# Performance work log

Measured on AMD Instinct MI355X. Metric: run time of the kernel, lower is better.

Reference implementation:

```python
import jax, jax.numpy as jnp
import numpy as np

B, N, F, T = 32, 2048, 64, 24


def setup_inputs() -> dict:
    key = jax.random.key(0)
    ks = jax.random.split(key, 6)
    x = jax.random.normal(ks[0], (B, N, F, T), dtype=jnp.float32)
    # glorot-uniform-ish init scales
    def glorot(k, shape):
        fan_in, fan_out = shape[-2], shape[-1]
        lim = (6.0 / (fan_in + fan_out)) ** 0.5
        return jax.random.uniform(k, shape, jnp.float32, -lim, lim)
    W1 = glorot(ks[1], (T, 1))
    W2 = glorot(ks[2], (F, T))
    W3 = glorot(ks[3], (1, F))
    bs = glorot(ks[4], (1, N, N))
    Vs = glorot(ks[5], (N, N))
    return {"x": x, "W1": W1, "W2": W2, "W3": W3, "bs": bs, "Vs": Vs}


def reference(x, W1, W2, W3, bs, Vs):
    # x: (B, N, F, T)
    # lhs = squeeze(x @ W1, -1) @ W2  -> (B, N, T)
    lhs = jnp.einsum('bnft,t->bnf', x, W1[:, 0])          # (B,N,F)
    lhs = jnp.einsum('bnf,ft->bnt', lhs, W2)              # (B,N,T)
    # rhs = transpose(squeeze(W3 @ x, 2), (0,2,1)) -> (B, T, N)
    rhs = jnp.einsum('f,bnft->btn', W3[0], x)             # (B,T,N)
    product = jnp.einsum('bnt,btm->bnm', lhs, rhs)        # (B,N,N)
    S = jnp.einsum('nk,bkm->bnm', Vs, jax.nn.sigmoid(product + bs))  # (B,N,N)
    # softmax over axis 1 (rows of the N x N map)
    return jax.nn.softmax(S, axis=1)
```

## Files before the change

kernel.cpp:

```cpp
#include <hip/hip_runtime.h>

constexpr int Bc = 32, Nc = 2048, Fc = 64, Tc = 24;

__device__ __forceinline__ unsigned short f2bf(float f) {
  unsigned u = __float_as_uint(f);
  u += 0x7fffu + ((u >> 16) & 1u);
  return (unsigned short)(u >> 16);
}

#define AS1(p) ((const __attribute__((address_space(1))) unsigned int*)(p))
#define AS3(p) ((__attribute__((address_space(3))) unsigned int*)(p))

typedef __attribute__((ext_vector_type(8))) short bfrag;
typedef __attribute__((ext_vector_type(4))) float ffrag;

__global__ __launch_bounds__(256) void kA(const float* __restrict__ x,
                                          const float* __restrict__ W1,
                                          const float* __restrict__ W2,
                                          const float* __restrict__ W3,
                                          float* __restrict__ lhs,
                                          float* __restrict__ rhsT) {
  __shared__ float W2s[Fc * Tc];
  __shared__ float xs[4][Fc][26];
  __shared__ float tmp[4][Fc];
  const int tid = threadIdx.x;
  for (int i = tid; i < Fc * Tc; i += 256) W2s[i] = W2[i];
  const int wave = tid >> 6, lane = tid & 63;
  const size_t pair = (size_t)blockIdx.x * 4 + wave;
  const float* xp = x + pair * (size_t)(Fc * Tc);
#pragma unroll
  for (int s = 0; s < 12; ++s) {
    int f2 = lane + 64 * s;
    int row = f2 / 12, c2 = (f2 % 12) * 2;
    float2 v = *(const float2*)(xp + (size_t)f2 * 2);
    xs[wave][row][c2] = v.x;
    xs[wave][row][c2 + 1] = v.y;
  }
  __syncthreads();
  {
    const int f = lane;
    float acc = 0.f;
#pragma unroll
    for (int t = 0; t < Tc; ++t) acc += xs[wave][f][t] * W1[t];
    tmp[wave][f] = acc;
  }
  __syncthreads();
  if (lane < 48) {
    const int t = lane >> 1, h = lane & 1;
    const int f0 = h * 32;
    float lacc = 0.f, racc = 0.f;
#pragma unroll
    for (int i = 0; i < 32; ++i) {
      int f = f0 + i;
      lacc += tmp[wave][f] * W2s[f * Tc + t];
      racc += W3[f] * xs[wave][f][t];
    }
    lacc += __shfl_xor(lacc, 1);
    racc += __shfl_xor(racc, 1);
    if (h == 0) {
      lhs[pair * Tc + t] = lacc;
      rhsT[pair * Tc + t] = racc;
    }
  }
}

__global__ __launch_bounds__(256) void kVs(const float* __restrict__ Vs,
                                           unsigned short* __restrict__ Vb) {
  size_t i = ((size_t)blockIdx.x * 256 + threadIdx.x) * 4;
  float4 v = *(const float4*)(Vs + i);
  ushort4 o;
  o.x = f2bf(v.x); o.y = f2bf(v.y); o.z = f2bf(v.z); o.w = f2bf(v.w);
  *(ushort4*)(Vb + i) = o;
}

__global__ __launch_bounds__(256) void kP(const float* __restrict__ lhs,
                                          const float* __restrict__ rhsT,
                                          const float* __restrict__ bsr,
                                          unsigned short* __restrict__ sigT) {
  __shared__ float Lt[Tc][132];
  __shared__ float Rt[Tc][132];
  const int b = blockIdx.z;
  const int i0 = blockIdx.y * 128;
  const int j0 = blockIdx.x * 128;
  const int tid = threadIdx.x;
  const float* lp = lhs + ((size_t)b * Nc + i0) * Tc;
  const float* rp = rhsT + ((size_t)b * Nc + j0) * Tc;
#pragma unroll
  for (int s = 0; s < 6; ++s) {
    int f2 = tid + 256 * s;
    int row = f2 / 12, c2 = (f2 % 12) * 2;
    float2 v = *(const float2*)(lp + (size_t)row * Tc + c2);
    Lt[c2][row] = v.x; Lt[c2 + 1][row] = v.y;
    float2 w = *(const float2*)(rp + (size_t)row * Tc + c2);
    Rt[c2][row] = w.x; Rt[c2 + 1][row] = w.y;
  }
  __syncthreads();
  const int tx = tid & 15, ty = tid >> 4;
  const int ri = ty * 8, cj = tx * 8;
  float acc[8][8];
#pragma unroll
  for (int a = 0; a < 8; ++a) {
    const float* bp = bsr + (size_t)(i0 + ri + a) * Nc + j0 + cj;
    float4 b0 = *(const float4*)bp;
    float4 b1 = *(const float4*)(bp + 4);
    acc[a][0] = b0.x; acc[a][1] = b0.y; acc[a][2] = b0.z; acc[a][3] = b0.w;
    acc[a][4] = b1.x; acc[a][5] = b1.y; acc[a][6] = b1.z; acc[a][7] = b1.w;
  }
#pragma unroll
  for (int t = 0; t < Tc; ++t) {
    float la[8], ra[8];
    *(float4*)&la[0] = *(const float4*)&Lt[t][ri];
    *(float4*)&la[4] = *(const float4*)&Lt[t][ri + 4];
    *(float4*)&ra[0] = *(const float4*)&Rt[t][cj];
    *(float4*)&ra[4] = *(const float4*)&Rt[t][cj + 4];
#pragma unroll
    for (int a = 0; a < 8; ++a)
#pragma unroll
      for (int c = 0; c < 8; ++c) acc[a][c] += la[a] * ra[c];
  }
#pragma unroll
  for (int c = 0; c < 8; ++c) {
    unsigned short o[8];
#pragma unroll
    for (int a = 0; a < 8; ++a) {
      float e = __expf(-acc[a][c]);
      o[a] = f2bf(__fdividef(1.0f, 1.0f + e));
    }
    uint4 pk;
    pk.x = (unsigned)o[0] | ((unsigned)o[1] << 16);
    pk.y = (unsigned)o[2] | ((unsigned)o[3] << 16);
    pk.z = (unsigned)o[4] | ((unsigned)o[5] << 16);
    pk.w = (unsigned)o[6] | ((unsigned)o[7] << 16);
    *(uint4*)(sigT + ((size_t)b * Nc + j0 + cj + c) * Nc + i0 + ri) = pk;
  }
}

__global__ __launch_bounds__(256) void kG(const unsigned short* __restrict__ A,
                                          const unsigned short* __restrict__ Bm,
                                          float* __restrict__ S) {
  __shared__ unsigned short As[128 * 32];
  __shared__ unsigned short Bs[128 * 32];
  const int b = blockIdx.y;
  const int n0 = (blockIdx.x >> 4) << 7;
  const int m0 = (blockIdx.x & 15) << 7;
  const int tid = threadIdx.x;
  const int wave = tid >> 6, lane = tid & 63;
  const int quad = lane >> 4, l16 = lane & 15;
  const int wrow = (wave >> 1) << 6, wcol = (wave & 1) << 6;
  const unsigned short* Bg = Bm + (size_t)b * Nc * Nc;

  ffrag acc[4][4];
#pragma unroll
  for (int i = 0; i < 4; ++i)
#pragma unroll
    for (int j = 0; j < 4; ++j) acc[i][j] = (ffrag){0.f, 0.f, 0.f, 0.f};

  const int part = (lane & 3) * 8;
  const int row0 = (wave << 4) + (lane >> 2);
  const int row1 = row0 + 64;

  for (int kt = 0; kt < Nc / 32; ++kt) {
    const int k0 = kt * 32;
    __builtin_amdgcn_global_load_lds(AS1(A + (size_t)(n0 + row0) * Nc + k0 + part),
                                     AS3(&As[(wave * 64) * 8]), 16, 0, 0);
    __builtin_amdgcn_global_load_lds(AS1(A + (size_t)(n0 + row1) * Nc + k0 + part),
                                     AS3(&As[(256 + wave * 64) * 8]), 16, 0, 0);
    __builtin_amdgcn_global_load_lds(AS1(Bg + (size_t)(m0 + row0) * Nc + k0 + part),
                                     AS3(&Bs[(wave * 64) * 8]), 16, 0, 0);
    __builtin_amdgcn_global_load_lds(AS1(Bg + (size_t)(m0 + row1) * Nc + k0 + part),
                                     AS3(&Bs[(256 + wave * 64) * 8]), 16, 0, 0);
    __syncthreads();
    bfrag af[4], bg[4];
#pragma unroll
    for (int mi = 0; mi < 4; ++mi)
      af[mi] = *(const bfrag*)&As[(wrow + mi * 16 + l16) * 32 + quad * 8];
#pragma unroll
    for (int ni = 0; ni < 4; ++ni)
      bg[ni] = *(const bfrag*)&Bs[(wcol + ni * 16 + l16) * 32 + quad * 8];
#pragma unroll
    for (int mi = 0; mi < 4; ++mi)
#pragma unroll
      for (int ni = 0; ni < 4; ++ni)
        acc[mi][ni] = __builtin_amdgcn_mfma_f32_16x16x32_bf16(af[mi], bg[ni], acc[mi][ni], 0, 0, 0);
    __syncthreads();
  }
  float* Sp = S + (size_t)b * Nc * Nc;
#pragma unroll
  for (int mi = 0; mi < 4; ++mi)
#pragma unroll
    for (int r = 0; r < 4; ++r) {
      const int row = n0 + wrow + mi * 16 + quad * 4 + r;
#pragma unroll
      for (int ni = 0; ni < 4; ++ni)
        Sp[(size_t)row * Nc + (m0 + wcol + ni * 16 + l16)] = acc[mi][ni][r];
    }
}

__global__ __launch_bounds__(256) void kS1(const float* __restrict__ S,
                                           float* __restrict__ pmax,
                                           float* __restrict__ psum) {
  const int b = blockIdx.z, mt = blockIdx.y, nc = blockIdx.x;
  const int m = mt * 256 + threadIdx.x;
  const float* col = S + (size_t)b * Nc * Nc + m;
  float mx = -3.0e38f, sm = 0.f;
  const int ns = nc * 512;
#pragma unroll 4
  for (int n = ns; n < ns + 512; ++n) {
    float v = col[(size_t)n * Nc];
    float nm = fmaxf(mx, v);
    sm = sm * __expf(mx - nm) + __expf(v - nm);
    mx = nm;
  }
  pmax[(size_t)(b * 4 + nc) * Nc + m] = mx;
  psum[(size_t)(b * 4 + nc) * Nc + m] = sm;
}

__global__ __launch_bounds__(256) void kS1b(const float* __restrict__ pmax,
                                            const float* __restrict__ psum,
                                            float* __restrict__ rmax,
                                            float* __restrict__ rinv) {
  const int i = blockIdx.x * 256 + threadIdx.x;
  const int b = i >> 11, m = i & 2047;
  const float* pm = pmax + (size_t)b * 4 * Nc + m;
  const float* ps = psum + (size_t)b * 4 * Nc + m;
  float gm = pm[0];
#pragma unroll
  for (int c = 1; c < 4; ++c) gm = fmaxf(gm, pm[(size_t)c * Nc]);
  float gs = 0.f;
#pragma unroll
  for (int c = 0; c < 4; ++c) gs += ps[(size_t)c * Nc] * __expf(pm[(size_t)c * Nc] - gm);
  rmax[i] = gm;
  rinv[i] = 1.0f / gs;
}

__global__ __launch_bounds__(256) void kS2(float* __restrict__ S,
                                           const float* __restrict__ rmax,
                                           const float* __restrict__ rinv) {
  const int b = blockIdx.z, mt = blockIdx.y, nc = blockIdx.x;
  const int m = mt * 256 + threadIdx.x;
  const float gm = rmax[b * Nc + m];
  const float iv = rinv[b * Nc + m];
  float* col = S + (size_t)b * Nc * Nc + m;
  const int ns = nc * 256;
#pragma unroll 4
  for (int n = ns; n < ns + 256; ++n) {
    float v = col[(size_t)n * Nc];
    col[(size_t)n * Nc] = __expf(v - gm) * iv;
  }
}

extern "C" void kernel_launch(void* const* d_in, const int* in_sizes, int n_in,
                              void* d_out, int out_size, void* d_ws, size_t ws_size,
                              hipStream_t stream) {
  const float* x   = (const float*)d_in[0];
  const float* W1  = (const float*)d_in[1];
  const float* W2  = (const float*)d_in[2];
  const float* W3  = (const float*)d_in[3];
  const float* bsr = (const float*)d_in[4];
  const float* Vs  = (const float*)d_in[5];
  float* out = (float*)d_out;

  char* ws = (char*)d_ws;
  constexpr size_t SIGT_B = (size_t)Bc * Nc * Nc * 2;
  constexpr size_t VB_B   = (size_t)Nc * Nc * 2;
  constexpr size_t LHS_B  = (size_t)Bc * Nc * Tc * 4;
  constexpr size_t PM_B   = (size_t)Bc * 4 * Nc * 4;
  unsigned short* sigT = (unsigned short*)ws;
  unsigned short* Vb   = (unsigned short*)(ws + SIGT_B);
  float* lhs  = (float*)(ws + SIGT_B + VB_B);
  float* rhsT = (float*)(ws + SIGT_B + VB_B + LHS_B);
  float* pmax = (float*)(ws + SIGT_B + VB_B + 2 * LHS_B);
  float* psum = (float*)(ws + SIGT_B + VB_B + 2 * LHS_B + PM_B);
  float* rmax = (float*)(ws + SIGT_B + VB_B + 2 * LHS_B + 2 * PM_B);
  float* rinv = (float*)(ws + SIGT_B + VB_B + 2 * LHS_B + 2 * PM_B + (size_t)Bc * Nc * 4);

  kA<<<Bc * Nc / 4, 256, 0, stream>>>(x, W1, W2, W3, lhs, rhsT);
  kVs<<<(Nc * Nc) / 1024, 256, 0, stream>>>(Vs, Vb);
  kP<<<dim3(Nc / 128, Nc / 128, Bc), 256, 0, stream>>>(lhs, rhsT, bsr, sigT);
  kG<<<dim3((Nc / 128) * (Nc / 128), Bc), 256, 0, stream>>>(Vb, sigT, out);
  kS1<<<dim3(4, Nc / 256, Bc), 256, 0, stream>>>(out, pmax, psum);
  kS1b<<<Bc * Nc / 256, 256, 0, stream>>>(pmax, psum, rmax, rinv);
  kS2<<<dim3(Nc / 256, Nc / 256, Bc), 256, 0, stream>>>(out, rmax, rinv);
}
```

Measured before the change: 2.195 ms.

## Rewrite batched bf16 GEMM as 256x256 double-buffered pipelined MFMA kernel

```diff
diff --git a/kernel.cpp b/kernel.cpp
--- a/kernel.cpp
+++ b/kernel.cpp
@@ -135,65 +135,166 @@
   }
 }
 
-__global__ __launch_bounds__(256) void kG(const unsigned short* __restrict__ A,
-                                          const unsigned short* __restrict__ Bm,
-                                          float* __restrict__ S) {
-  __shared__ unsigned short As[128 * 32];
-  __shared__ unsigned short Bs[128 * 32];
+__global__ __launch_bounds__(512, 2) void kG(const unsigned short* __restrict__ A,
+                                             const unsigned short* __restrict__ Bm,
+                                             float* __restrict__ S) {
+  __shared__ unsigned short As[2][2][8192];
+  __shared__ unsigned short Bs[2][2][8192];
   const int b = blockIdx.y;
-  const int n0 = (blockIdx.x >> 4) << 7;
-  const int m0 = (blockIdx.x & 15) << 7;
+  const int bid = blockIdx.x;
+  const int swz = (bid & 7) * 8 + (bid >> 3);
+  const int n0 = (swz >> 3) << 8;
+  const int m0 = (swz & 7) << 8;
   const int tid = threadIdx.x;
-  const int wave = tid >> 6, lane = tid & 63;
+  const int wid = tid >> 6, lane = tid & 63;
+  const int wm = wid >> 2, wn = wid & 3;
   const int quad = lane >> 4, l16 = lane & 15;
-  const int wrow = (wave >> 1) << 6, wcol = (wave & 1) << 6;
   const unsigned short* Bg = Bm + (size_t)b * Nc * Nc;
 
-  ffrag acc[4][4];
-#pragma unroll
-  for (int i = 0; i < 4; ++i)
-#pragma unroll
-    for (int j = 0; j < 4; ++j) acc[i][j] = (ffrag){0.f, 0.f, 0.f, 0.f};
-
-  const int part = (lane & 3) * 8;
-  const int row0 = (wave << 4) + (lane >> 2);
-  const int row1 = row0 + 64;
-
-  for (int kt = 0; kt < Nc / 32; ++kt) {
-    const int k0 = kt * 32;
-    __builtin_amdgcn_global_load_lds(AS1(A + (size_t)(n0 + row0) * Nc + k0 + part),
-                                     AS3(&As[(wave * 64) * 8]), 16, 0, 0);
-    __builtin_amdgcn_global_load_lds(AS1(A + (size_t)(n0 + row1) * Nc + k0 + part),
-                                     AS3(&As[(256 + wave * 64) * 8]), 16, 0, 0);
-    __builtin_amdgcn_global_load_lds(AS1(Bg + (size_t)(m0 + row0) * Nc + k0 + part),
-                                     AS3(&Bs[(wave * 64) * 8]), 16, 0, 0);
-    __builtin_amdgcn_global_load_lds(AS1(Bg + (size_t)(m0 + row1) * Nc + k0 + part),
-                                     AS3(&Bs[(256 + wave * 64) * 8]), 16, 0, 0);
-    __syncthreads();
-    bfrag af[4], bg[4];
+  int srow[2], scol[2], sbase[2];
+#pragma unroll
+  for (int c = 0; c < 2; ++c) {
+    const int d = c * 8192 + (wid << 10) + (lane << 4);
+    const int q = d ^ (((d >> 9) & 1) << 5);
+    srow[c] = q >> 7;
+    scol[c] = (q & 127) >> 1;
+    sbase[c] = (c * 8192 + (wid << 10)) >> 1;
+  }
+
+#define STAGE(arr, bufb, half, gb, ro, k0)                                         \
+  do {                                                                             \
+    _Pragma("unroll")                                                              \
+    for (int c = 0; c < 2; ++c)                                                    \
+      __builtin_amdgcn_global_load_lds(                                            \
+          AS1(gb + (size_t)((ro) + srow[c]) * Nc + (k0) + scol[c]),                \
+          AS3(&arr[bufb][half][0] + sbase[c]), 16, 0, 0);                          \
+  } while (0)
+
+  ffrag acc[2][4][2][2];
+#pragma unroll
+  for (int qm = 0; qm < 2; ++qm)
 #pragma unroll
     for (int mi = 0; mi < 4; ++mi)
-      af[mi] = *(const bfrag*)&As[(wrow + mi * 16 + l16) * 32 + quad * 8];
-#pragma unroll
-    for (int ni = 0; ni < 4; ++ni)
-      bg[ni] = *(const bfrag*)&Bs[(wcol + ni * 16 + l16) * 32 + quad * 8];
+#pragma unroll
+      for (int qn = 0; qn < 2; ++qn)
+#pragma unroll
+        for (int ni = 0; ni < 2; ++ni) acc[qm][mi][qn][ni] = (ffrag){0.f, 0.f, 0.f, 0.f};
+
+  bfrag af[4][2], bfr[2][2];
+
+#define LDA(qm, bufb)                                                              \
+  do {                                                                             \
+    _Pragma("unroll")                                                              \
+    for (int mi = 0; mi < 4; ++mi)                                                 \
+      _Pragma("unroll")                                                            \
+      for (int ks = 0; ks < 2; ++ks) {                                             \
+        const int lin = (wm * 64 + mi * 16 + l16) * 128 + ks * 64 + quad * 16;     \
+        const int ph = lin ^ (((lin >> 9) & 1) << 5);                              \
+        af[mi][ks] = *(const bfrag*)((const char*)&As[bufb][qm][0] + ph);          \
+      }                                                                            \
+  } while (0)
+
+#define LDB(qn, bufb)                                                              \
+  do {                                                                             \
+    _Pragma("unroll")                                                              \
+    for (int ni = 0; ni < 2; ++ni)                                                 \
+      _Pragma("unroll")                                                            \
+      for (int ks = 0; ks < 2; ++ks) {                                             \
+        const int lin = (wn * 32 + ni * 16 + l16) * 128 + ks * 64 + quad * 16;     \
+        const int ph = lin ^ (((lin >> 9) & 1) << 5);                              \
+        bfr[ni][ks] = *(const bfrag*)((const char*)&Bs[bufb][qn][0] + ph);         \
+      }                                                                            \
+  } while (0)
+
+#define MM(qm, qn)                                                                 \
+  do {                                                                             \
+    __builtin_amdgcn_s_setprio(1);                                                 \
+    _Pragma("unroll")                                                              \
+    for (int mi = 0; mi < 4; ++mi)                                                 \
+      _Pragma("unroll")                                                            \
+      for (int ni = 0; ni < 2; ++ni)                                               \
+        _Pragma("unroll")                                                          \
+        for (int ks = 0; ks < 2; ++ks)                                             \
+          acc[qm][mi][qn][ni] = __builtin_amdgcn_mfma_f32_16x16x32_bf16(           \
+              af[mi][ks], bfr[ni][ks], acc[qm][mi][qn][ni], 0, 0, 0);              \
+    __builtin_amdgcn_s_setprio(0);                                                 \
+  } while (0)
+
+#define TILE(BUF, OT, T, DO_S1, DO_S2, ENDW)                                       \
+  do {                                                                             \
+    const int k1 = ((T) + 1) << 6, k2 = ((T) + 2) << 6;                            \
+                                                      \
+    LDA(0, BUF); LDB(0, BUF);                                                      \
+    if (DO_S1) STAGE(Bs, OT, 0, Bg, m0, k1);                                       \
+    asm volatile("s_waitcnt lgkmcnt(8)");                                          \
+    __builtin_amdgcn_s_barrier();                                                  \
+    asm volatile("s_waitcnt lgkmcnt(0)");                                          \
+    MM(0, 0);                                                                      \
+    __builtin_amdgcn_s_barrier();                                                  \
+                                     \
+    LDB(1, BUF);                                                                   \
+    if (DO_S2) STAGE(As, BUF, 0, A, n0, k2);                                       \
+    __builtin_amdgcn_s_barrier();                                                  \
+    asm volatile("s_waitcnt lgkmcnt(0)");                                          \
+    MM(0, 1);                                                                      \
+    __builtin_amdgcn_s_barrier();                                                  \
+                                     \
+    LDA(1, BUF);                                                                   \
+    if (DO_S2) STAGE(Bs, BUF, 1, Bg, m0 + 128, k2);                                \
+    __builtin_amdgcn_s_barrier();                                                  \
+    asm volatile("s_waitcnt lgkmcnt(0)");                                          \
+    MM(1, 1);                                                                      \
+    __builtin_amdgcn_s_barrier();                                                  \
+                                                      \
+    LDB(0, BUF);                                                                   \
+    if (DO_S2) STAGE(As, BUF, 1, A, n0 + 128, k2);                                 \
+    __builtin_amdgcn_s_barrier();                                                  \
+    asm volatile("s_waitcnt lgkmcnt(0)");                                          \
+    MM(1, 0);                                                                      \
+    ENDW;                                                                          \
+    __builtin_amdgcn_s_barrier();                                                  \
+  } while (0)
+
+  constexpr int NT = Nc / 64;
+  STAGE(As, 0, 0, A,  n0,       0);
+  STAGE(Bs, 0, 1, Bg, m0 + 128, 0);
+  STAGE(As, 0, 1, A,  n0 + 128, 0);
+  STAGE(Bs, 0, 0, Bg, m0,       0);
+  asm volatile("s_waitcnt vmcnt(4)" ::: "memory");
+  STAGE(As, 1, 0, A,  n0,       64);
+  STAGE(Bs, 1, 1, Bg, m0 + 128, 64);
+  STAGE(As, 1, 1, A,  n0 + 128, 64);
+  asm volatile("s_waitcnt vmcnt(6)" ::: "memory");
+  __builtin_amdgcn_s_barrier();
+
+  for (int t = 0; t < NT - 2; t += 2) {
+    TILE(0, 1, t,     true, true, asm volatile("s_waitcnt vmcnt(6)" ::: "memory"));
+    TILE(1, 0, t + 1, true, true, asm volatile("s_waitcnt vmcnt(6)" ::: "memory"));
+  }
+  TILE(0, 1, NT - 2, true,  false, asm volatile("s_waitcnt vmcnt(0)" ::: "memory"));
+  TILE(1, 0, NT - 1, false, false, (void)0);
+
+#undef TILE
+#undef MM
+#undef LDB
+#undef LDA
+#undef STAGE
+
+  float* Sp = S + (size_t)b * Nc * Nc;
+#pragma unroll
+  for (int qm = 0; qm < 2; ++qm)
 #pragma unroll
     for (int mi = 0; mi < 4; ++mi)
 #pragma unroll
-      for (int ni = 0; ni < 4; ++ni)
-        acc[mi][ni] = __builtin_amdgcn_mfma_f32_16x16x32_bf16(af[mi], bg[ni], acc[mi][ni], 0, 0, 0);
-    __syncthreads();
-  }
-  float* Sp = S + (size_t)b * Nc * Nc;
-#pragma unroll
-  for (int mi = 0; mi < 4; ++mi)
-#pragma unroll
-    for (int r = 0; r < 4; ++r) {
-      const int row = n0 + wrow + mi * 16 + quad * 4 + r;
-#pragma unroll
-      for (int ni = 0; ni < 4; ++ni)
-        Sp[(size_t)row * Nc + (m0 + wcol + ni * 16 + l16)] = acc[mi][ni][r];
-    }
+      for (int r = 0; r < 4; ++r) {
+        const int row = n0 + qm * 128 + wm * 64 + mi * 16 + quad * 4 + r;
+#pragma unroll
+        for (int qn = 0; qn < 2; ++qn)
+#pragma unroll
+          for (int ni = 0; ni < 2; ++ni)
+            Sp[(size_t)row * Nc + (m0 + qn * 128 + wn * 32 + ni * 16 + l16)] =
+                acc[qm][mi][qn][ni][r];
+      }
 }
 
 __global__ __launch_bounds__(256) void kS1(const float* __restrict__ S,
@@ -277,7 +378,7 @@
   kA<<<Bc * Nc / 4, 256, 0, stream>>>(x, W1, W2, W3, lhs, rhsT);
   kVs<<<(Nc * Nc) / 1024, 256, 0, stream>>>(Vs, Vb);
   kP<<<dim3(Nc / 128, Nc / 128, Bc), 256, 0, stream>>>(lhs, rhsT, bsr, sigT);
-  kG<<<dim3((Nc / 128) * (Nc / 128), Bc), 256, 0, stream>>>(Vb, sigT, out);
+  kG<<<dim3((Nc / 256) * (Nc / 256), Bc), 512, 0, stream>>>(Vb, sigT, out);
   kS1<<<dim3(4, Nc / 256, Bc), 256, 0, stream>>>(out, pmax, psum);
   kS1b<<<Bc * Nc / 256, 256, 0, stream>>>(pmax, psum, rmax, rinv);
   kS2<<<dim3(Nc / 256, Nc / 256, Bc), 256, 0, stream>>>(out, rmax, rinv);
```

Measured after the change: 1.879 ms. -14.4%, faster.
